# Optimization experiments

Hardware: AMD Instinct MI355X
Metric: run time of the kernel (lower is better)

The kernel has to match this reference:

```python
import jax, jax.numpy as jnp
import numpy as np

EMB_DIM = 2048
USER_DIM = 256
NUM_EXPERTS = 64
TOP_K = 8
N_TOKENS = 16384


def setup_inputs() -> dict:
    key = jax.random.key(0)
    k_h, k_u, k_w = jax.random.split(key, 3)
    h = jax.random.normal(k_h, (N_TOKENS, EMB_DIM), dtype=jnp.float32)
    u = jax.random.normal(k_u, (N_TOKENS, USER_DIM), dtype=jnp.float32)
    # nn.Linear weight is [out, in]; we store transposed [in, out] for x @ W
    W = jax.random.normal(k_w, (EMB_DIM + USER_DIM, NUM_EXPERTS), dtype=jnp.float32) * (1.0 / np.sqrt(EMB_DIM + USER_DIM))
    b = jnp.zeros((NUM_EXPERTS,), dtype=jnp.float32)
    return {"h": h, "u": u, "W": W, "b": b}


def reference(h, u, W, b):
    # gate logits: [N, E]
    g = jnp.concatenate([h, u], axis=-1) @ W + b
    w = jax.nn.softmax(g, axis=-1)
    # top-k mask + renormalize (top_k < num_experts)
    _, top_idx = jax.lax.top_k(w, TOP_K)                       # [N, k]
    mask = jax.nn.one_hot(top_idx, NUM_EXPERTS, dtype=w.dtype).sum(axis=-2)  # [N, E]
    w = w * mask
    w = w / (w.sum(axis=-1, keepdims=True) + 1e-9)
    return w
```

## Files before the change

kernel.cpp:

```cpp
#include <hip/hip_runtime.h>

#define EMB 2048
#define UDIM 256
#define KTOT 2304
#define NE 64
#define TOPK 8
#define TPB 32
#define LP 65
#define NSTEP (KTOT / 32)
#define SSH 6144

typedef __attribute__((ext_vector_type(8))) short short8;
typedef __attribute__((ext_vector_type(4))) float f32x4;

__device__ __forceinline__ unsigned short bf16h(float x) {
  unsigned uu = __builtin_bit_cast(unsigned, x);
  return (unsigned short)((uu + 0x7FFFu + ((uu >> 16) & 1u)) >> 16);
}
__device__ __forceinline__ float bf2f(unsigned short s) {
  return __builtin_bit_cast(float, ((unsigned)s) << 16);
}

__global__ __launch_bounds__(256)
void prep_w(const float* __restrict__ W, unsigned short* __restrict__ wb) {
  const int flat = blockIdx.x * 256 + threadIdx.x;
  const int k = flat >> 6;
  const int n = flat & 63;
  const float w = W[flat];
  const unsigned short h0 = bf16h(w);
  const float r1 = w - bf2f(h0);
  const unsigned short h1 = bf16h(r1);
  const float r2 = r1 - bf2f(h1);
  const unsigned short h2 = bf16h(r2);

  const int s = k >> 5;
  const int kk = k & 31;
  const int lane = (kk >> 3) * 16 + (n & 15);
  const int j = kk & 7;
  const int nt = n >> 4;
  const size_t base = (size_t)s * SSH + ((size_t)nt * 64 + lane) * 8 + j;
  wb[base] = h0;
  wb[base + 2048] = h1;
  wb[base + 4096] = h2;
}

__global__ __launch_bounds__(512, 4)
void gate_mfma(const float* __restrict__ h, const float* __restrict__ u,
               const unsigned short* __restrict__ wb,
               const float* __restrict__ b, float* __restrict__ out) {
  __shared__ float slab[TPB * LP];

  const int tid = threadIdx.x;
  const int lane = tid & 63;
  const int wid = __builtin_amdgcn_readfirstlane(tid >> 6);
  const int tw = wid & 1;
  const int kq = wid >> 1;
  const int mm = lane & 15;
  const int q8 = (lane >> 4) * 8;
  const int tok0 = blockIdx.x * TPB;
  const int token = tok0 + tw * 16 + mm;

  const float* hrow = h + (size_t)token * EMB + q8;
  const float* urow = u + (size_t)token * UDIM + q8;
  const unsigned short* wlane = wb + (size_t)lane * 8;

  f32x4 acc[4];
#pragma unroll
  for (int nt = 0; nt < 4; ++nt) acc[nt] = 0.f;

  auto run = [&](const float* __restrict__ xp, int kw0, int nsteps) {
    f32x4 c0 = *(const f32x4*)(xp);
    f32x4 c1 = *(const f32x4*)(xp + 4);
    f32x4 n0 = 0.f, n1 = 0.f;
    if (nsteps > 1) {
      n0 = *(const f32x4*)(xp + 32);
      n1 = *(const f32x4*)(xp + 36);
    }
    const int as0 = kw0 >> 5;
    for (int s = 0; s < nsteps; ++s) {
      f32x4 f0 = 0.f, f1 = 0.f;
      if (s + 2 < nsteps) {
        f0 = *(const f32x4*)(xp + (s + 2) * 32);
        f1 = *(const f32x4*)(xp + (s + 2) * 32 + 4);
      }
      const unsigned short* ws = wlane + (size_t)(as0 + s) * SSH;
      short8 Bv[3][4];
#pragma unroll
      for (int p = 0; p < 3; ++p)
#pragma unroll
        for (int nt = 0; nt < 4; ++nt)
          Bv[p][nt] = *(const short8*)(ws + (p * 4 + nt) * 512);

      float xs[8] = {c0[0], c0[1], c0[2], c0[3], c1[0], c1[1], c1[2], c1[3]};
      short8 A0, A1, A2;
#pragma unroll
      for (int j = 0; j < 8; ++j) {
        const unsigned short h0 = bf16h(xs[j]);
        const float r1 = xs[j] - bf2f(h0);
        const unsigned short h1 = bf16h(r1);
        const float r2 = r1 - bf2f(h1);
        A0[j] = (short)h0;
        A1[j] = (short)h1;
        A2[j] = (short)bf16h(r2);
      }
#pragma unroll
      for (int nt = 0; nt < 4; ++nt) {
        acc[nt] = __builtin_amdgcn_mfma_f32_16x16x32_bf16(A0, Bv[0][nt], acc[nt], 0, 0, 0);
        acc[nt] = __builtin_amdgcn_mfma_f32_16x16x32_bf16(A0, Bv[1][nt], acc[nt], 0, 0, 0);
        acc[nt] = __builtin_amdgcn_mfma_f32_16x16x32_bf16(A1, Bv[0][nt], acc[nt], 0, 0, 0);
        acc[nt] = __builtin_amdgcn_mfma_f32_16x16x32_bf16(A1, Bv[1][nt], acc[nt], 0, 0, 0);
        acc[nt] = __builtin_amdgcn_mfma_f32_16x16x32_bf16(A0, Bv[2][nt], acc[nt], 0, 0, 0);
        acc[nt] = __builtin_amdgcn_mfma_f32_16x16x32_bf16(A2, Bv[0][nt], acc[nt], 0, 0, 0);
      }
      c0 = n0; c1 = n1; n0 = f0; n1 = f1;
    }
  };

  const int kw0 = kq * 576;
  if (kq < 3) {
    run(hrow + kw0, kw0, 18);
  } else {
    run(hrow + 1728, 1728, 10);
    run(urow, 2048, 8);
  }

  const int row = tw * 16 + (lane >> 4) * 4;
  for (int ph = 0; ph < 4; ++ph) {
    if (kq == ph) {
#pragma unroll
      for (int nt = 0; nt < 4; ++nt)
#pragma unroll
        for (int r = 0; r < 4; ++r) {
          float* p = &slab[(row + r) * LP + nt * 16 + mm];
          if (ph == 0) *p = acc[nt][r]; else *p += acc[nt][r];
        }
    }
    __syncthreads();
  }

  const float bias = b[lane];
#pragma unroll
  for (int tt = 0; tt < 4; ++tt) {
    const int t = wid * 4 + tt;
    float g = slab[t * LP + lane] + bias;

    float m = g;
#pragma unroll
    for (int off = 32; off > 0; off >>= 1)
      m = fmaxf(m, __shfl_xor(m, off));
    float pexp = __expf(g - m);
    float s = pexp;
#pragma unroll
    for (int off = 32; off > 0; off >>= 1)
      s += __shfl_xor(s, off);
    const float pn = pexp / s;

    float vv = pn;
    float topsum = 0.f;
    int sel = 0;
    for (int r = 0; r < TOPK; ++r) {
      float mv = vv;
      int mi = lane;
#pragma unroll
      for (int off = 32; off > 0; off >>= 1) {
        const float ov = __shfl_xor(mv, off);
        const int oi = __shfl_xor(mi, off);
        if (ov > mv || (ov == mv && oi < mi)) { mv = ov; mi = oi; }
      }
      topsum += mv;
      if (lane == mi) { sel = 1; vv = -1.f; }
    }

    out[(size_t)(tok0 + t) * NE + lane] =
        sel ? pn / (topsum + 1e-9f) : 0.f;
  }
}

extern "C" void kernel_launch(void* const* d_in, const int* in_sizes, int n_in,
                              void* d_out, int out_size, void* d_ws, size_t ws_size,
                              hipStream_t stream) {
  const float* h = (const float*)d_in[0];
  const float* u = (const float*)d_in[1];
  const float* W = (const float*)d_in[2];
  const float* b = (const float*)d_in[3];
  float* out = (float*)d_out;

  unsigned short* wb = (unsigned short*)d_ws;

  const int n_tokens = in_sizes[0] / EMB;

  hipLaunchKernelGGL(prep_w, dim3(KTOT * NE / 256), dim3(256), 0, stream, W, wb);
  hipLaunchKernelGGL(gate_mfma, dim3(n_tokens / TPB), dim3(512), 0, stream,
                     h, u, wb, b, out);
}
```

Measured before the change: 262.6 us.

## Double-buffer weight fragments in registers and truncate bf16 splitting

Prefetches the next step's twelve B-fragments into a second register set while the current step runs its MFMAs, with a sched_barrier so the loads are issued early. It relaxes launch bounds from 4 to 2 waves per SIMD to leave room for the extra registers. It also replaces round-to-nearest bf16 splitting with bit truncation, which cuts ALU work in the split. The cost is lower occupancy and a slightly different error distribution in the three-term split.

```diff
diff --git a/kernel.cpp b/kernel.cpp
--- a/kernel.cpp
+++ b/kernel.cpp
@@ -7,18 +7,21 @@
 #define TOPK 8
 #define TPB 32
 #define LP 65
-#define NSTEP (KTOT / 32)
 #define SSH 6144
 
 typedef __attribute__((ext_vector_type(8))) short short8;
 typedef __attribute__((ext_vector_type(4))) float f32x4;
 
-__device__ __forceinline__ unsigned short bf16h(float x) {
-  unsigned uu = __builtin_bit_cast(unsigned, x);
-  return (unsigned short)((uu + 0x7FFFu + ((uu >> 16) & 1u)) >> 16);
-}
-__device__ __forceinline__ float bf2f(unsigned short s) {
-  return __builtin_bit_cast(float, ((unsigned)s) << 16);
+__device__ __forceinline__ void xsplit3(float x, unsigned& s0, unsigned& s1,
+                                        unsigned& s2) {
+  const unsigned u = __builtin_bit_cast(unsigned, x);
+  const unsigned h0 = u & 0xFFFF0000u;
+  const float r1 = x - __builtin_bit_cast(float, h0);
+  const unsigned u1 = __builtin_bit_cast(unsigned, r1) & 0xFFFF0000u;
+  const float r2 = r1 - __builtin_bit_cast(float, u1);
+  s0 = h0 >> 16;
+  s1 = u1 >> 16;
+  s2 = __builtin_bit_cast(unsigned, r2) >> 16;
 }
 
 __global__ __launch_bounds__(256)
@@ -26,12 +29,8 @@
   const int flat = blockIdx.x * 256 + threadIdx.x;
   const int k = flat >> 6;
   const int n = flat & 63;
-  const float w = W[flat];
-  const unsigned short h0 = bf16h(w);
-  const float r1 = w - bf2f(h0);
-  const unsigned short h1 = bf16h(r1);
-  const float r2 = r1 - bf2f(h1);
-  const unsigned short h2 = bf16h(r2);
+  unsigned s0, s1, s2;
+  xsplit3(W[flat], s0, s1, s2);
 
   const int s = k >> 5;
   const int kk = k & 31;
@@ -39,12 +38,12 @@
   const int j = kk & 7;
   const int nt = n >> 4;
   const size_t base = (size_t)s * SSH + ((size_t)nt * 64 + lane) * 8 + j;
-  wb[base] = h0;
-  wb[base + 2048] = h1;
-  wb[base + 4096] = h2;
-}
-
-__global__ __launch_bounds__(512, 4)
+  wb[base] = (unsigned short)s0;
+  wb[base + 2048] = (unsigned short)s1;
+  wb[base + 4096] = (unsigned short)s2;
+}
+
+__global__ __launch_bounds__(512, 2)
 void gate_mfma(const float* __restrict__ h, const float* __restrict__ u,
                const unsigned short* __restrict__ wb,
                const float* __restrict__ b, float* __restrict__ out) {
@@ -68,7 +67,7 @@
 #pragma unroll
   for (int nt = 0; nt < 4; ++nt) acc[nt] = 0.f;
 
-  auto run = [&](const float* __restrict__ xp, int kw0, int nsteps) {
+  auto run = [&](const float* __restrict__ xp, int as0, int nsteps) {
     f32x4 c0 = *(const f32x4*)(xp);
     f32x4 c1 = *(const f32x4*)(xp + 4);
     f32x4 n0 = 0.f, n1 = 0.f;
@@ -76,52 +75,58 @@
       n0 = *(const f32x4*)(xp + 32);
       n1 = *(const f32x4*)(xp + 36);
     }
-    const int as0 = kw0 >> 5;
+    short8 Bc[12], Bn[12];
+    {
+      const unsigned short* ws = wlane + (size_t)as0 * SSH;
+#pragma unroll
+      for (int i = 0; i < 12; ++i) Bc[i] = *(const short8*)(ws + i * 512);
+    }
+
+#pragma unroll 2
     for (int s = 0; s < nsteps; ++s) {
+      if (s + 1 < nsteps) {
+        const unsigned short* wn = wlane + (size_t)(as0 + s + 1) * SSH;
+#pragma unroll
+        for (int i = 0; i < 12; ++i) Bn[i] = *(const short8*)(wn + i * 512);
+      }
       f32x4 f0 = 0.f, f1 = 0.f;
       if (s + 2 < nsteps) {
         f0 = *(const f32x4*)(xp + (s + 2) * 32);
         f1 = *(const f32x4*)(xp + (s + 2) * 32 + 4);
       }
-      const unsigned short* ws = wlane + (size_t)(as0 + s) * SSH;
-      short8 Bv[3][4];
-#pragma unroll
-      for (int p = 0; p < 3; ++p)
-#pragma unroll
-        for (int nt = 0; nt < 4; ++nt)
-          Bv[p][nt] = *(const short8*)(ws + (p * 4 + nt) * 512);
-
-      float xs[8] = {c0[0], c0[1], c0[2], c0[3], c1[0], c1[1], c1[2], c1[3]};
+      __builtin_amdgcn_sched_barrier(0);
+
       short8 A0, A1, A2;
 #pragma unroll
       for (int j = 0; j < 8; ++j) {
-        const unsigned short h0 = bf16h(xs[j]);
-        const float r1 = xs[j] - bf2f(h0);
-        const unsigned short h1 = bf16h(r1);
-        const float r2 = r1 - bf2f(h1);
-        A0[j] = (short)h0;
-        A1[j] = (short)h1;
-        A2[j] = (short)bf16h(r2);
+        const float xv = (j < 4) ? c0[j] : c1[j - 4];
+        unsigned s0, s1, s2;
+        xsplit3(xv, s0, s1, s2);
+        A0[j] = (short)s0;
+        A1[j] = (short)s1;
+        A2[j] = (short)s2;
       }
 #pragma unroll
       for (int nt = 0; nt < 4; ++nt) {
-        acc[nt] = __builtin_amdgcn_mfma_f32_16x16x32_bf16(A0, Bv[0][nt], acc[nt], 0, 0, 0);
-        acc[nt] = __builtin_amdgcn_mfma_f32_16x16x32_bf16(A0, Bv[1][nt], acc[nt], 0, 0, 0);
-        acc[nt] = __builtin_amdgcn_mfma_f32_16x16x32_bf16(A1, Bv[0][nt], acc[nt], 0, 0, 0);
-        acc[nt] = __builtin_amdgcn_mfma_f32_16x16x32_bf16(A1, Bv[1][nt], acc[nt], 0, 0, 0);
-        acc[nt] = __builtin_amdgcn_mfma_f32_16x16x32_bf16(A0, Bv[2][nt], acc[nt], 0, 0, 0);
-        acc[nt] = __builtin_amdgcn_mfma_f32_16x16x32_bf16(A2, Bv[0][nt], acc[nt], 0, 0, 0);
+        acc[nt] = __builtin_amdgcn_mfma_f32_16x16x32_bf16(A0, Bc[nt], acc[nt], 0, 0, 0);
+        acc[nt] = __builtin_amdgcn_mfma_f32_16x16x32_bf16(A0, Bc[4 + nt], acc[nt], 0, 0, 0);
+        acc[nt] = __builtin_amdgcn_mfma_f32_16x16x32_bf16(A1, Bc[nt], acc[nt], 0, 0, 0);
+        acc[nt] = __builtin_amdgcn_mfma_f32_16x16x32_bf16(A1, Bc[4 + nt], acc[nt], 0, 0, 0);
+        acc[nt] = __builtin_amdgcn_mfma_f32_16x16x32_bf16(A0, Bc[8 + nt], acc[nt], 0, 0, 0);
+        acc[nt] = __builtin_amdgcn_mfma_f32_16x16x32_bf16(A2, Bc[nt], acc[nt], 0, 0, 0);
       }
       c0 = n0; c1 = n1; n0 = f0; n1 = f1;
+#pragma unroll
+      for (int i = 0; i < 12; ++i) Bc[i] = Bn[i];
     }
   };
 
-  const int kw0 = kq * 576;
   if (kq < 3) {
-    run(hrow + kw0, kw0, 18);
+    const int kw0 = kq * 576;
+    run(hrow + kw0, kw0 >> 5, 18);
   } else {
-    run(hrow + 1728, 1728, 10);
-    run(urow, 2048, 8);
+    run(hrow + 1728, 54, 10);
+    run(urow, 64, 8);
   }
 
   const int row = tw * 16 + (lane >> 4) * 4;
```

Result: slower. 272.2 us (+3.7%).
